# Performance work log

Measured on AMD Instinct MI355X. Metric: run time of the kernel, lower is better.

## Reference

```python
import jax, jax.numpy as jnp
import numpy as np

N_NODES = 20000
N_EDGES = 640000
IN_DIM = 128
HID = 128
NUM_GRAPHS = 64


def setup_inputs() -> dict:
    key = jax.random.key(0)
    ks = jax.random.split(key, 12)
    x = jax.random.normal(ks[0], (N_NODES, IN_DIM), dtype=jnp.float32)
    edge_index = jax.random.randint(ks[1], (2, N_EDGES), 0, N_NODES, dtype=jnp.int64)
    batch = jnp.sort(jax.random.randint(ks[2], (N_NODES,), 0, NUM_GRAPHS, dtype=jnp.int64))
    edge_attr = jax.random.uniform(ks[3], (N_EDGES,), dtype=jnp.float32)
    s1 = 1.0 / np.sqrt(IN_DIM)
    s2 = 1.0 / np.sqrt(HID)
    # GraphConv layer 1: lin_rel (with bias) on aggregated messages, lin_root (no bias) on x
    W1_rel = jax.random.uniform(ks[4], (HID, IN_DIM), minval=-s1, maxval=s1, dtype=jnp.float32)
    b1 = jax.random.uniform(ks[5], (HID,), minval=-s1, maxval=s1, dtype=jnp.float32)
    W1_root = jax.random.uniform(ks[6], (HID, IN_DIM), minval=-s1, maxval=s1, dtype=jnp.float32)
    # GraphConv layer 3 (conv2 is unused in forward)
    W3_rel = jax.random.uniform(ks[7], (HID, HID), minval=-s2, maxval=s2, dtype=jnp.float32)
    b3 = jax.random.uniform(ks[8], (HID,), minval=-s2, maxval=s2, dtype=jnp.float32)
    W3_root = jax.random.uniform(ks[9], (HID, HID), minval=-s2, maxval=s2, dtype=jnp.float32)
    # Final linear head
    Wlin = jax.random.uniform(ks[10], (1, HID), minval=-s2, maxval=s2, dtype=jnp.float32)
    blin = jax.random.uniform(ks[11], (1,), minval=-s2, maxval=s2, dtype=jnp.float32)
    return {
        "x": x, "edge_index": edge_index, "batch": batch, "edge_attr": edge_attr,
        "W1_rel": W1_rel, "b1": b1, "W1_root": W1_root,
        "W3_rel": W3_rel, "b3": b3, "W3_root": W3_root,
        "Wlin": Wlin, "blin": blin, "num_graphs": NUM_GRAPHS,
    }


def graph_conv(x, src, dst, edge_w, W_rel, b_rel, W_root):
    # PyG GraphConv (aggr='add'): out = W_rel @ sum_{j in N(i)} w_ij * x_j + b_rel + W_root @ x_i
    msg = x[src] * edge_w[:, None]                       # [E, d] gather + scale
    agg = jax.ops.segment_sum(msg, dst, num_segments=x.shape[0])  # [N, d] scatter-add
    return agg @ W_rel.T + b_rel + x @ W_root.T


def reference(x, edge_index, batch, edge_attr,
              W1_rel, b1, W1_root, W3_rel, b3, W3_root, Wlin, blin, num_graphs):
    src, dst = edge_index[0], edge_index[1]
    h = graph_conv(x, src, dst, edge_attr, W1_rel, b1, W1_root)
    h = jax.nn.relu(h)
    # dropout p=0.5 is identity in eval mode
    h = graph_conv(h, src, dst, edge_attr, W3_rel, b3, W3_root)
    # global_mean_pool over per-node graph ids
    sums = jax.ops.segment_sum(h, batch, num_segments=num_graphs)          # [G, H]
    counts = jax.ops.segment_sum(jnp.ones((h.shape[0],), h.dtype), batch,
                                 num_segments=num_graphs)                  # [G]
    pooled = sums / jnp.maximum(counts, 1.0)[:, None]
    out = jax.nn.relu(pooled @ Wlin.T + blin)                              # [G, 1]
    return out
```

## Files before the change

kernel.cpp:

```cpp
#include <hip/hip_runtime.h>

#define N_NODES 20000
#define N_EDGES 640000
#define DIM 128
#define NGRAPH 64
#define NBUCK 313
#define CAP 2560
#define EPB 1024
#define NB_PART 625
#define NB_WCONV 32
#define NB_GEMM 1252
#define RED_BLOCKS 512

typedef __attribute__((ext_vector_type(8))) short short8;
typedef __attribute__((ext_vector_type(4))) float floatx4;

__device__ __forceinline__ unsigned int bf16rne(float f) {
    unsigned int u = __float_as_uint(f);
    return (u + 0x7FFFu + ((u >> 16) & 1u)) >> 16;
}

__global__ __launch_bounds__(256) void k_part_prep(
    const int* __restrict__ src, const int* __restrict__ dst,
    const float* __restrict__ ew,
    const float* __restrict__ W1rel, const float* __restrict__ W1root,
    const float* __restrict__ W3rel, const float* __restrict__ W3root,
    const float* __restrict__ b3, const float* __restrict__ Wlin,
    int* __restrict__ gcursor, int2* __restrict__ part,
    unsigned short* __restrict__ wbh, unsigned short* __restrict__ wbl,
    float* __restrict__ vrel, float* __restrict__ vroot, float* __restrict__ cb3) {

    const int t = threadIdx.x;
    const int blk = blockIdx.x;

    if (blk < NB_PART) {
        __shared__ int lhist[NBUCK], lbase[NBUCK], gbase[NBUCK], lcur[NBUCK];
        __shared__ int2 lrec[EPB];
        for (int i = t; i < NBUCK; i += 256) lhist[i] = 0;
        __syncthreads();
        const int e0 = blk * EPB;
        const int tot = min(EPB, N_EDGES - e0);
        int mys[4], myd[4];
        float myw[4];
        for (int i = 0; i < 4; ++i) {
            int e = e0 + i * 256 + t;
            if (e < N_EDGES) {
                mys[i] = src[e];
                myd[i] = dst[e];
                myw[i] = ew[e];
                atomicAdd(&lhist[myd[i] >> 6], 1);
            } else {
                myd[i] = -1;
            }
        }
        __syncthreads();
        if (t < 64) {
            int carry = 0;
            for (int c = 0; c < 5; ++c) {
                int idx = c * 64 + t;
                int v = (idx < NBUCK) ? lhist[idx] : 0;
                int xv = v;
                for (int s = 1; s < 64; s <<= 1) {
                    int u = __shfl_up(xv, s);
                    if (t >= s) xv += u;
                }
                if (idx < NBUCK) { lbase[idx] = carry + xv - v; lcur[idx] = 0; }
                carry += __shfl(xv, 63);
            }
        }
        __syncthreads();
        for (int i = t; i < NBUCK; i += 256) {
            int cnt = lhist[i];
            gbase[i] = cnt ? (i * CAP + atomicAdd(&gcursor[i], cnt)) : 0;
        }
        __syncthreads();
        for (int i = 0; i < 4; ++i) {
            if (myd[i] >= 0) {
                int bb = myd[i] >> 6;
                int slot = lbase[bb] + atomicAdd(&lcur[bb], 1);
                lrec[slot] = make_int2((myd[i] << 16) | mys[i], __float_as_int(myw[i]));
            }
        }
        __syncthreads();
        for (int i = t; i < tot; i += 256) {
            int2 rc = lrec[i];
            int bb = ((unsigned)rc.x >> 16) >> 6;
            part[gbase[bb] + (i - lbase[bb])] = rc;
        }
    } else if (blk < NB_PART + NB_WCONV) {
        const int b = blk - NB_PART;
        for (int i = b * 256 + t; i < 256 * DIM; i += NB_WCONV * 256) {
            int n = i >> 7, k = i & 127;
            float v = (n < DIM) ? W1rel[n * DIM + k] : W1root[(n - DIM) * DIM + k];
            unsigned int h = bf16rne(v);
            wbh[i] = (unsigned short)h;
            wbl[i] = (unsigned short)bf16rne(v - __uint_as_float(h << 16));
        }
    } else {
        if (t < 64) {
            for (int kk = 0; kk < 2; ++kk) {
                int k = t + kk * 64;
                float sr = 0.f, so = 0.f;
                for (int h = 0; h < DIM; ++h) {
                    float wl = Wlin[h];
                    sr = fmaf(wl, W3rel[h * DIM + k], sr);
                    so = fmaf(wl, W3root[h * DIM + k], so);
                }
                vrel[k] = sr;
                vroot[k] = so;
            }
            float c = b3[t] * Wlin[t] + b3[t + 64] * Wlin[t + 64];
            for (int m = 32; m > 0; m >>= 1) c += __shfl_xor(c, m);
            if (t == 0) cb3[0] = c;
        }
    }
}

union SMem2 {
    struct { int2 lrec[CAP]; int nh[64], ncur[64]; } s;
    struct { unsigned short h[64 * DIM], l[64 * DIM]; } g;
};

__global__ __launch_bounds__(256) void k_sort_gemm(
    const int* __restrict__ gcursor, int2* __restrict__ part,
    int* __restrict__ off, int* __restrict__ nend,
    const float* __restrict__ x,
    const unsigned short* __restrict__ wbh, const unsigned short* __restrict__ wbl,
    const float* __restrict__ b1,
    unsigned short* __restrict__ yb, float* __restrict__ r) {
    __shared__ SMem2 sm;
    const int t = threadIdx.x;

    if (blockIdx.x < NBUCK) {
        const int b = blockIdx.x;
        const int base = b * CAP;
        const int cnt = gcursor[b];
        for (int i = t; i < cnt; i += 256) sm.s.lrec[i] = part[base + i];
        if (t < 64) sm.s.nh[t] = 0;
        __syncthreads();
        for (int i = t; i < cnt; i += 256)
            atomicAdd(&sm.s.nh[((unsigned)sm.s.lrec[i].x >> 16) & 63], 1);
        __syncthreads();
        if (t < 64) {
            int v = sm.s.nh[t];
            int xv = v;
            for (int s = 1; s < 64; s <<= 1) {
                int u = __shfl_up(xv, s);
                if (t >= s) xv += u;
            }
            int excl = xv - v;
            sm.s.ncur[t] = excl;
            int node = b * 64 + t;
            if (node < N_NODES) {
                off[node] = base + excl;
                nend[node] = base + excl + v;
            }
        }
        __syncthreads();
        for (int i = t; i < cnt; i += 256) {
            int2 rc = sm.s.lrec[i];
            int dl = ((unsigned)rc.x >> 16) & 63;
            int p = atomicAdd(&sm.s.ncur[dl], 1);
            part[base + p] = make_int2(rc.x & 0xFFFF, rc.y);
        }
    } else {
        const int tile = blockIdx.x - NBUCK;
        const int g = tile >> 2;
        const int col0 = (tile & 3) * 64;
        uint4* sh = (uint4*)sm.g.h;
        uint4* sl = (uint4*)sm.g.l;
        const uint4* gh = (const uint4*)wbh + (size_t)col0 * 16;
        const uint4* gl = (const uint4*)wbl + (size_t)col0 * 16;
        for (int i = t; i < 1024; i += 256) {
            int row = i >> 4, c = i & 15;
            int sc = row * 16 + (c ^ (row & 15));
            sh[sc] = gh[i];
            sl[sc] = gl[i];
        }
        __syncthreads();

        const int lane = t & 63;
        const int m = lane & 15;
        const int q = lane >> 4;
        const int row0 = g * 64 + (t >> 6) * 16;
        const int row = row0 + m;
        const bool ok = row < N_NODES;
        const short8* SH = (const short8*)sm.g.h;
        const short8* SL = (const short8*)sm.g.l;

        floatx4 acc[4];
        #pragma unroll
        for (int i = 0; i < 4; ++i) acc[i] = (floatx4)(0.f);

        #pragma unroll
        for (int kc = 0; kc < 4; ++kc) {
            float4 v0 = make_float4(0.f, 0.f, 0.f, 0.f);
            float4 v1 = make_float4(0.f, 0.f, 0.f, 0.f);
            if (ok) {
                const float4* xp = (const float4*)(x + (size_t)row * DIM + kc * 32 + q * 8);
                v0 = xp[0];
                v1 = xp[1];
            }
            float f[8] = {v0.x, v0.y, v0.z, v0.w, v1.x, v1.y, v1.z, v1.w};
            short8 ah, al;
            #pragma unroll
            for (int i = 0; i < 8; ++i) {
                unsigned int h = bf16rne(f[i]);
                ah[i] = (short)h;
                al[i] = (short)bf16rne(f[i] - __uint_as_float(h << 16));
            }
            #pragma unroll
            for (int nt = 0; nt < 4; ++nt) {
                int nl = nt * 16 + m;
                int cc = (kc * 4 + q) ^ m;
                short8 bh = SH[nl * 16 + cc];
                short8 bl = SL[nl * 16 + cc];
                acc[nt] = __builtin_amdgcn_mfma_f32_16x16x32_bf16(ah, bh, acc[nt], 0, 0, 0);
                acc[nt] = __builtin_amdgcn_mfma_f32_16x16x32_bf16(al, bh, acc[nt], 0, 0, 0);
                acc[nt] = __builtin_amdgcn_mfma_f32_16x16x32_bf16(ah, bl, acc[nt], 0, 0, 0);
            }
        }

        #pragma unroll
        for (int nt = 0; nt < 4; ++nt) {
            int col = col0 + nt * 16 + m;
            float bias = (col >= DIM) ? b1[col - DIM] : 0.f;
            #pragma unroll
            for (int reg = 0; reg < 4; ++reg) {
                int orow = row0 + q * 4 + reg;
                if (orow < N_NODES) {
                    float v = acc[nt][reg];
                    if (col < DIM)
                        yb[orow * DIM + col] = (unsigned short)bf16rne(v);
                    else
                        r[orow * DIM + (col - DIM)] = v + bias;
                }
            }
        }
    }
}

__global__ __launch_bounds__(256) void k_agg(const unsigned int* __restrict__ yb,
                                             const float2* __restrict__ r2,
                                             const int* __restrict__ off,
                                             const int* __restrict__ nend,
                                             const int2* __restrict__ grec,
                                             const float2* __restrict__ vrel2,
                                             const float2* __restrict__ vroot2,
                                             float* __restrict__ aout,
                                             float* __restrict__ bout) {
    const int lane = threadIdx.x & 63;
    const int node = blockIdx.x * 4 + (threadIdx.x >> 6);
    if (node >= N_NODES) return;

    int j = off[node];
    const int e1 = nend[node];
    float sx = 0.f, sy = 0.f;
    for (; j + 8 <= e1; j += 8) {
        int2 rc[8];
        #pragma unroll
        for (int u = 0; u < 8; ++u) rc[u] = grec[j + u];
        unsigned int v[8];
        #pragma unroll
        for (int u = 0; u < 8; ++u) v[u] = yb[rc[u].x * 64 + lane];
        #pragma unroll
        for (int u = 0; u < 8; ++u) {
            float w = __int_as_float(rc[u].y);
            sx = fmaf(w, __uint_as_float(v[u] << 16), sx);
            sy = fmaf(w, __uint_as_float(v[u] & 0xFFFF0000u), sy);
        }
    }
    for (; j < e1; ++j) {
        int2 rcs = grec[j];
        float w = __int_as_float(rcs.y);
        unsigned int vv = yb[rcs.x * 64 + lane];
        sx = fmaf(w, __uint_as_float(vv << 16), sx);
        sy = fmaf(w, __uint_as_float(vv & 0xFFFF0000u), sy);
    }
    float2 rr = r2[(size_t)node * 64 + lane];
    float hx = fmaxf(sx + rr.x, 0.f);
    float hy = fmaxf(sy + rr.y, 0.f);
    float2 vr = vrel2[lane];
    float2 vo = vroot2[lane];
    float pa = hx * vr.x + hy * vr.y;
    float pb = hx * vo.x + hy * vo.y;
    for (int mm = 32; mm > 0; mm >>= 1) {
        pa += __shfl_xor(pa, mm);
        pb += __shfl_xor(pb, mm);
    }
    if (lane == 0) {
        aout[node] = pa;
        bout[node] = pb;
    }
}

__global__ __launch_bounds__(256) void k_reduce_final(
    const int2* __restrict__ grec, const int* __restrict__ off,
    const int* __restrict__ nend,
    const float* __restrict__ a, const float* __restrict__ bvec,
    const int* __restrict__ batch,
    float* __restrict__ gpart, int* __restrict__ gpartc,
    int* __restrict__ ticket_red,
    const float* __restrict__ cb3, const float* __restrict__ blin,
    float* __restrict__ out) {
    __shared__ float sbin[NGRAPH];
    __shared__ int cbin[NGRAPH];
    __shared__ int islast;
    const int t = threadIdx.x;
    for (int i = t; i < NGRAPH; i += 256) { sbin[i] = 0.f; cbin[i] = 0; }
    __syncthreads();
    const int lane = t & 63;
    const int gw = blockIdx.x * 4 + (t >> 6);
    const int nw = gridDim.x * 4;
    for (int node = gw; node < N_NODES; node += nw) {
        const int e0 = off[node], e1 = nend[node];
        float s = 0.f;
        for (int j = e0 + lane; j < e1; j += 64) {
            int2 rc = grec[j];
            s = fmaf(__int_as_float(rc.y), a[rc.x], s);
        }
        for (int mm = 32; mm > 0; mm >>= 1) s += __shfl_xor(s, mm);
        if (lane == 0) {
            int g = batch[node];
            atomicAdd(&sbin[g], s + bvec[node]);
            atomicAdd(&cbin[g], 1);
        }
    }
    __syncthreads();
    const int slot = blockIdx.x & 63;
    for (int i = t; i < NGRAPH; i += 256) {
        atomicAdd(&gpart[slot * NGRAPH + i], sbin[i]);
        if (cbin[i]) atomicAdd(&gpartc[slot * NGRAPH + i], cbin[i]);
    }
    __syncthreads();
    if (t == 0) {
        __threadfence();
        islast = (atomicAdd(ticket_red, 1) == (int)gridDim.x - 1);
    }
    __syncthreads();
    if (islast) {
        __threadfence();
        if (t < NGRAPH) {
            float S = 0.f;
            int C = 0;
            for (int s2 = 0; s2 < 64; ++s2) {
                S += __hip_atomic_load(&gpart[s2 * NGRAPH + t], __ATOMIC_RELAXED,
                                       __HIP_MEMORY_SCOPE_AGENT);
                C += __hip_atomic_load(&gpartc[s2 * NGRAPH + t], __ATOMIC_RELAXED,
                                       __HIP_MEMORY_SCOPE_AGENT);
            }
            float denom = (C > 0) ? (float)C : 1.f;
            float v = (S + (float)C * cb3[0]) / denom + blin[0];
            out[t] = (v > 0.f) ? v : 0.f;
        }
    }
}

extern "C" void kernel_launch(void* const* d_in, const int* in_sizes, int n_in,
                              void* d_out, int out_size, void* d_ws, size_t ws_size,
                              hipStream_t stream) {
    const float* x = (const float*)d_in[0];
    const int* edge_index = (const int*)d_in[1];
    const int* src = edge_index;
    const int* dst = edge_index + N_EDGES;
    const int* batch = (const int*)d_in[2];
    const float* ew = (const float*)d_in[3];
    const float* W1rel = (const float*)d_in[4];
    const float* b1 = (const float*)d_in[5];
    const float* W1root = (const float*)d_in[6];
    const float* W3rel = (const float*)d_in[7];
    const float* b3 = (const float*)d_in[8];
    const float* W3root = (const float*)d_in[9];
    const float* Wlin = (const float*)d_in[10];
    const float* blin = (const float*)d_in[11];
    float* out = (float*)d_out;

    char* w = (char*)d_ws;
    size_t o = 0;
    auto alloc = [&](size_t bytes) -> void* {
        void* p = w + o;
        o += bytes;
        o = (o + 255) & ~(size_t)255;
        return p;
    };
    char* zbase = (char*)alloc((NBUCK + 1) * 4 + 64 * NGRAPH * 4 * 2);
    int* gcursor = (int*)zbase;
    int* ticket_red = gcursor + NBUCK;
    float* gpart = (float*)(zbase + (NBUCK + 1) * 4);
    int* gpartc = (int*)(zbase + (NBUCK + 1) * 4 + 64 * NGRAPH * 4);
    const size_t zbytes = (NBUCK + 1) * 4 + 64 * NGRAPH * 4 * 2;

    unsigned short* wbh = (unsigned short*)alloc((size_t)256 * DIM * 2);
    unsigned short* wbl = (unsigned short*)alloc((size_t)256 * DIM * 2);
    unsigned short* yb = (unsigned short*)alloc((size_t)N_NODES * DIM * 2);
    float* r = (float*)alloc((size_t)N_NODES * DIM * 4);
    int2* part = (int2*)alloc((size_t)NBUCK * CAP * 8);
    int* off = (int*)alloc((size_t)N_NODES * 4);
    int* nend = (int*)alloc((size_t)N_NODES * 4);
    float* a = (float*)alloc((size_t)N_NODES * 4);
    float* b = (float*)alloc((size_t)N_NODES * 4);
    float* vrel = (float*)alloc(DIM * 4);
    float* vroot = (float*)alloc(DIM * 4);
    float* cb3 = (float*)alloc(4);

    hipMemsetAsync(zbase, 0, zbytes, stream);

    k_part_prep<<<NB_PART + NB_WCONV + 1, 256, 0, stream>>>(
        src, dst, ew, W1rel, W1root, W3rel, W3root, b3, Wlin,
        gcursor, part, wbh, wbl, vrel, vroot, cb3);

    k_sort_gemm<<<NBUCK + NB_GEMM, 256, 0, stream>>>(
        gcursor, part, off, nend, x, wbh, wbl, b1, yb, r);

    k_agg<<<(N_NODES + 3) / 4, 256, 0, stream>>>(
        (const unsigned int*)yb, (const float2*)r, off, nend, part,
        (const float2*)vrel, (const float2*)vroot, a, b);

    k_reduce_final<<<RED_BLOCKS, 256, 0, stream>>>(
        part, off, nend, a, b, batch, gpart, gpartc, ticket_red, cb3, blin, out);
}
```

Before: 181.6 us.

## Aggregate raw bf16 features before layer-1 GEMM and fuse the dot reductions

New measurement: 222.6 us. 22.6% more time.

```diff
diff --git a/kernel.cpp b/kernel.cpp
--- a/kernel.cpp
+++ b/kernel.cpp
@@ -8,9 +8,8 @@
 #define CAP 2560
 #define EPB 1024
 #define NB_PART 625
+#define NB_XCONV 160
 #define NB_WCONV 32
-#define NB_GEMM 1252
-#define RED_BLOCKS 512
 
 typedef __attribute__((ext_vector_type(8))) short short8;
 typedef __attribute__((ext_vector_type(4))) float floatx4;
@@ -20,15 +19,27 @@
     return (u + 0x7FFFu + ((u >> 16) & 1u)) >> 16;
 }
 
+__device__ __forceinline__ int lowerb(const int* __restrict__ arr, int n, int v) {
+    int lo = 0, hi = n;
+    while (lo < hi) {
+        int mid = (lo + hi) >> 1;
+        if (arr[mid] < v) lo = mid + 1; else hi = mid;
+    }
+    return lo;
+}
+
 __global__ __launch_bounds__(256) void k_part_prep(
     const int* __restrict__ src, const int* __restrict__ dst,
-    const float* __restrict__ ew,
+    const float* __restrict__ ew, const float* __restrict__ x,
+    const int* __restrict__ batch,
     const float* __restrict__ W1rel, const float* __restrict__ W1root,
     const float* __restrict__ W3rel, const float* __restrict__ W3root,
     const float* __restrict__ b3, const float* __restrict__ Wlin,
     int* __restrict__ gcursor, int2* __restrict__ part,
+    unsigned int* __restrict__ xb32,
     unsigned short* __restrict__ wbh, unsigned short* __restrict__ wbl,
-    float* __restrict__ vrel, float* __restrict__ vroot, float* __restrict__ cb3) {
+    float* __restrict__ vrel, float* __restrict__ vroot, float* __restrict__ cb3,
+    int* __restrict__ cntg) {
 
     const int t = threadIdx.x;
     const int blk = blockIdx.x;
@@ -70,8 +81,8 @@
         }
         __syncthreads();
         for (int i = t; i < NBUCK; i += 256) {
-            int cnt = lhist[i];
-            gbase[i] = cnt ? (i * CAP + atomicAdd(&gcursor[i], cnt)) : 0;
+            int c = lhist[i];
+            gbase[i] = c ? (i * CAP + atomicAdd(&gcursor[i], c)) : 0;
         }
         __syncthreads();
         for (int i = 0; i < 4; ++i) {
@@ -87,8 +98,19 @@
             int bb = ((unsigned)rc.x >> 16) >> 6;
             part[gbase[bb] + (i - lbase[bb])] = rc;
         }
-    } else if (blk < NB_PART + NB_WCONV) {
+    } else if (blk < NB_PART + NB_XCONV) {
         const int b = blk - NB_PART;
+        const float4* x4 = (const float4*)x;
+        uint2* xh2 = (uint2*)xb32;
+        for (int i = b * 256 + t; i < N_NODES * 32; i += NB_XCONV * 256) {
+            float4 v = x4[i];
+            uint2 hp;
+            hp.x = bf16rne(v.x) | (bf16rne(v.y) << 16);
+            hp.y = bf16rne(v.z) | (bf16rne(v.w) << 16);
+            xh2[i] = hp;
+        }
+    } else if (blk < NB_PART + NB_XCONV + NB_WCONV) {
+        const int b = blk - (NB_PART + NB_XCONV);
         for (int i = b * 256 + t; i < 256 * DIM; i += NB_WCONV * 256) {
             int n = i >> 7, k = i & 127;
             float v = (n < DIM) ? W1rel[n * DIM + k] : W1root[(n - DIM) * DIM + k];
@@ -109,6 +131,7 @@
                 vrel[k] = sr;
                 vroot[k] = so;
             }
+            cntg[t] = lowerb(batch, N_NODES, t + 1) - lowerb(batch, N_NODES, t);
             float c = b3[t] * Wlin[t] + b3[t + 64] * Wlin[t + 64];
             for (int m = 32; m > 0; m >>= 1) c += __shfl_xor(c, m);
             if (t == 0) cb3[0] = c;
@@ -116,243 +139,241 @@
     }
 }
 
-union SMem2 {
-    struct { int2 lrec[CAP]; int nh[64], ncur[64]; } s;
-    struct { unsigned short h[64 * DIM], l[64 * DIM]; } g;
-};
-
-__global__ __launch_bounds__(256) void k_sort_gemm(
-    const int* __restrict__ gcursor, int2* __restrict__ part,
-    int* __restrict__ off, int* __restrict__ nend,
-    const float* __restrict__ x,
+__global__ __launch_bounds__(256) void k_zgather(
+    const int* __restrict__ gcursor, const int2* __restrict__ part,
+    const unsigned int* __restrict__ xb32, float* __restrict__ z) {
+    __shared__ int2 lrec[4][256];
+    __shared__ int lcur[4];
+    const int t = threadIdx.x;
+    const int w = t >> 6;
+    const int lane = t & 63;
+    const int nodeBase = blockIdx.x * 4;
+    const int bucket = nodeBase >> 6;
+
+    if (t < 4) lcur[t] = 0;
+    __syncthreads();
+    const int base = bucket * CAP;
+    const int cnt = min(gcursor[bucket], CAP);
+    for (int i = t; i < cnt; i += 256) {
+        int2 rc = part[base + i];
+        int wi = (int)((unsigned)rc.x >> 16) - nodeBase;
+        if ((unsigned)wi < 4u) {
+            int s = atomicAdd(&lcur[wi], 1);
+            if (s < 256) lrec[wi][s] = rc;
+        }
+    }
+    __syncthreads();
+
+    const int node = nodeBase + w;
+    if (node >= N_NODES) return;
+    const int len = min(lcur[w], 256);
+    float sx = 0.f, sy = 0.f;
+    int j = 0;
+    for (; j + 8 <= len; j += 8) {
+        int2 rc[8];
+        #pragma unroll
+        for (int u = 0; u < 8; ++u) rc[u] = lrec[w][j + u];
+        unsigned int v[8];
+        #pragma unroll
+        for (int u = 0; u < 8; ++u) v[u] = xb32[(size_t)(rc[u].x & 0xFFFF) * 64 + lane];
+        #pragma unroll
+        for (int u = 0; u < 8; ++u) {
+            float ww = __int_as_float(rc[u].y);
+            sx = fmaf(ww, __uint_as_float(v[u] << 16), sx);
+            sy = fmaf(ww, __uint_as_float(v[u] & 0xFFFF0000u), sy);
+        }
+    }
+    for (; j < len; ++j) {
+        int2 rc = lrec[w][j];
+        float ww = __int_as_float(rc.y);
+        unsigned int vv = xb32[(size_t)(rc.x & 0xFFFF) * 64 + lane];
+        sx = fmaf(ww, __uint_as_float(vv << 16), sx);
+        sy = fmaf(ww, __uint_as_float(vv & 0xFFFF0000u), sy);
+    }
+    float2* z2 = (float2*)z;
+    z2[(size_t)node * 64 + lane] = make_float2(sx, sy);
+}
+
+__global__ __launch_bounds__(256) void k_gemm_dots(
+    const float* __restrict__ x, const float* __restrict__ z,
     const unsigned short* __restrict__ wbh, const unsigned short* __restrict__ wbl,
     const float* __restrict__ b1,
-    unsigned short* __restrict__ yb, float* __restrict__ r) {
-    __shared__ SMem2 sm;
+    const float* __restrict__ vrel, const float* __restrict__ vroot,
+    const int* __restrict__ batch,
+    float* __restrict__ aArr, float* __restrict__ gsum) {
+    __shared__ unsigned short smem[2][128 * 32];
     const int t = threadIdx.x;
-
-    if (blockIdx.x < NBUCK) {
-        const int b = blockIdx.x;
-        const int base = b * CAP;
-        const int cnt = gcursor[b];
-        for (int i = t; i < cnt; i += 256) sm.s.lrec[i] = part[base + i];
-        if (t < 64) sm.s.nh[t] = 0;
-        __syncthreads();
-        for (int i = t; i < cnt; i += 256)
-            atomicAdd(&sm.s.nh[((unsigned)sm.s.lrec[i].x >> 16) & 63], 1);
-        __syncthreads();
-        if (t < 64) {
-            int v = sm.s.nh[t];
-            int xv = v;
-            for (int s = 1; s < 64; s <<= 1) {
-                int u = __shfl_up(xv, s);
-                if (t >= s) xv += u;
+    const int g = blockIdx.x;
+    const int c0 = blockIdx.y * 64;
+
+    const int lane = t & 63;
+    const int m = lane & 15;
+    const int q = lane >> 4;
+    const int row0 = g * 64 + (t >> 6) * 16;
+
+    floatx4 acc[4];
+    #pragma unroll
+    for (int i = 0; i < 4; ++i) acc[i] = (floatx4)(0.f);
+
+    uint4* sh4 = (uint4*)smem[0];
+    uint4* sl4 = (uint4*)smem[1];
+    const uint4* gh = (const uint4*)wbh;
+    const uint4* gl = (const uint4*)wbl;
+
+    for (int kc = 0; kc < 4; ++kc) {
+        __syncthreads();
+        for (int i = t; i < 512; i += 256) {
+            int row = i >> 2, ch = i & 3;
+            int wbrow = (row < 64) ? (c0 + row) : (128 + c0 + row - 64);
+            int sc = row * 4 + (ch ^ ((row >> 2) & 3));
+            int gi = wbrow * 16 + kc * 4 + ch;
+            sh4[sc] = gh[gi];
+            sl4[sc] = gl[gi];
+        }
+        __syncthreads();
+
+        const int arow = row0 + m;
+        const bool ok = arow < N_NODES;
+        const float* zp = z + (size_t)arow * DIM + kc * 32 + q * 8;
+        float4 z0 = ((const float4*)zp)[0];
+        float4 z1 = ((const float4*)zp)[1];
+        float4 x0 = make_float4(0.f, 0.f, 0.f, 0.f);
+        float4 x1 = make_float4(0.f, 0.f, 0.f, 0.f);
+        if (ok) {
+            const float* xp = x + (size_t)arow * DIM + kc * 32 + q * 8;
+            x0 = ((const float4*)xp)[0];
+            x1 = ((const float4*)xp)[1];
+        }
+        float zf[8] = {z0.x, z0.y, z0.z, z0.w, z1.x, z1.y, z1.z, z1.w};
+        float xf[8] = {x0.x, x0.y, x0.z, x0.w, x1.x, x1.y, x1.z, x1.w};
+        short8 zh, zl, xh, xl;
+        #pragma unroll
+        for (int i = 0; i < 8; ++i) {
+            unsigned int h = bf16rne(zf[i]);
+            zh[i] = (short)h;
+            zl[i] = (short)bf16rne(zf[i] - __uint_as_float(h << 16));
+            unsigned int h2 = bf16rne(xf[i]);
+            xh[i] = (short)h2;
+            xl[i] = (short)bf16rne(xf[i] - __uint_as_float(h2 << 16));
+        }
+
+        const short8* SH = (const short8*)smem[0];
+        const short8* SL = (const short8*)smem[1];
+        #pragma unroll
+        for (int nt = 0; nt < 4; ++nt) {
+            int rrel = nt * 16 + m;
+            int rroot = 64 + nt * 16 + m;
+            int cc1 = q ^ ((rrel >> 2) & 3);
+            int cc2 = q ^ ((rroot >> 2) & 3);
+            short8 bh = SH[rrel * 4 + cc1];
+            short8 bl = SL[rrel * 4 + cc1];
+            short8 ch = SH[rroot * 4 + cc2];
+            short8 cl = SL[rroot * 4 + cc2];
+            acc[nt] = __builtin_amdgcn_mfma_f32_16x16x32_bf16(zh, bh, acc[nt], 0, 0, 0);
+            acc[nt] = __builtin_amdgcn_mfma_f32_16x16x32_bf16(zl, bh, acc[nt], 0, 0, 0);
+            acc[nt] = __builtin_amdgcn_mfma_f32_16x16x32_bf16(zh, bl, acc[nt], 0, 0, 0);
+            acc[nt] = __builtin_amdgcn_mfma_f32_16x16x32_bf16(xh, ch, acc[nt], 0, 0, 0);
+            acc[nt] = __builtin_amdgcn_mfma_f32_16x16x32_bf16(xl, ch, acc[nt], 0, 0, 0);
+            acc[nt] = __builtin_amdgcn_mfma_f32_16x16x32_bf16(xh, cl, acc[nt], 0, 0, 0);
+        }
+    }
+
+    float pa[4] = {0.f, 0.f, 0.f, 0.f};
+    float pb[4] = {0.f, 0.f, 0.f, 0.f};
+    #pragma unroll
+    for (int nt = 0; nt < 4; ++nt) {
+        int col = c0 + nt * 16 + m;
+        float vb = b1[col];
+        float vr = vrel[col];
+        float vo = vroot[col];
+        #pragma unroll
+        for (int reg = 0; reg < 4; ++reg) {
+            float h = fmaxf(acc[nt][reg] + vb, 0.f);
+            pa[reg] = fmaf(h, vr, pa[reg]);
+            pb[reg] = fmaf(h, vo, pb[reg]);
+        }
+    }
+    #pragma unroll
+    for (int reg = 0; reg < 4; ++reg) {
+        for (int mask = 1; mask < 16; mask <<= 1) {
+            pa[reg] += __shfl_xor(pa[reg], mask);
+            pb[reg] += __shfl_xor(pb[reg], mask);
+        }
+    }
+    const int g_lo = batch[min(g * 64, N_NODES - 1)];
+    const int g_hi = batch[min(g * 64 + 63, N_NODES - 1)];
+    float s_lo = 0.f, s_hi = 0.f;
+    if (m == 0) {
+        #pragma unroll
+        for (int reg = 0; reg < 4; ++reg) {
+            int row = row0 + q * 4 + reg;
+            if (row < N_NODES) {
+                atomicAdd(&aArr[row], pa[reg]);
+                if (batch[row] == g_lo) s_lo += pb[reg];
+                else s_hi += pb[reg];
             }
-            int excl = xv - v;
-            sm.s.ncur[t] = excl;
-            int node = b * 64 + t;
-            if (node < N_NODES) {
-                off[node] = base + excl;
-                nend[node] = base + excl + v;
-            }
-        }
-        __syncthreads();
-        for (int i = t; i < cnt; i += 256) {
-            int2 rc = sm.s.lrec[i];
-            int dl = ((unsigned)rc.x >> 16) & 63;
-            int p = atomicAdd(&sm.s.ncur[dl], 1);
-            part[base + p] = make_int2(rc.x & 0xFFFF, rc.y);
-        }
-    } else {
-        const int tile = blockIdx.x - NBUCK;
-        const int g = tile >> 2;
-        const int col0 = (tile & 3) * 64;
-        uint4* sh = (uint4*)sm.g.h;
-        uint4* sl = (uint4*)sm.g.l;
-        const uint4* gh = (const uint4*)wbh + (size_t)col0 * 16;
-        const uint4* gl = (const uint4*)wbl + (size_t)col0 * 16;
-        for (int i = t; i < 1024; i += 256) {
-            int row = i >> 4, c = i & 15;
-            int sc = row * 16 + (c ^ (row & 15));
-            sh[sc] = gh[i];
-            sl[sc] = gl[i];
-        }
-        __syncthreads();
-
-        const int lane = t & 63;
-        const int m = lane & 15;
-        const int q = lane >> 4;
-        const int row0 = g * 64 + (t >> 6) * 16;
-        const int row = row0 + m;
-        const bool ok = row < N_NODES;
-        const short8* SH = (const short8*)sm.g.h;
-        const short8* SL = (const short8*)sm.g.l;
-
-        floatx4 acc[4];
-        #pragma unroll
-        for (int i = 0; i < 4; ++i) acc[i] = (floatx4)(0.f);
-
-        #pragma unroll
-        for (int kc = 0; kc < 4; ++kc) {
-            float4 v0 = make_float4(0.f, 0.f, 0.f, 0.f);
-            float4 v1 = make_float4(0.f, 0.f, 0.f, 0.f);
-            if (ok) {
-                const float4* xp = (const float4*)(x + (size_t)row * DIM + kc * 32 + q * 8);
-                v0 = xp[0];
-                v1 = xp[1];
-            }
-            float f[8] = {v0.x, v0.y, v0.z, v0.w, v1.x, v1.y, v1.z, v1.w};
-            short8 ah, al;
-            #pragma unroll
-            for (int i = 0; i < 8; ++i) {
-                unsigned int h = bf16rne(f[i]);
-                ah[i] = (short)h;
-                al[i] = (short)bf16rne(f[i] - __uint_as_float(h << 16));
-            }
-            #pragma unroll
-            for (int nt = 0; nt < 4; ++nt) {
-                int nl = nt * 16 + m;
-                int cc = (kc * 4 + q) ^ m;
-                short8 bh = SH[nl * 16 + cc];
-                short8 bl = SL[nl * 16 + cc];
-                acc[nt] = __builtin_amdgcn_mfma_f32_16x16x32_bf16(ah, bh, acc[nt], 0, 0, 0);
-                acc[nt] = __builtin_amdgcn_mfma_f32_16x16x32_bf16(al, bh, acc[nt], 0, 0, 0);
-                acc[nt] = __builtin_amdgcn_mfma_f32_16x16x32_bf16(ah, bl, acc[nt], 0, 0, 0);
-            }
-        }
-
-        #pragma unroll
-        for (int nt = 0; nt < 4; ++nt) {
-            int col = col0 + nt * 16 + m;
-            float bias = (col >= DIM) ? b1[col - DIM] : 0.f;
-            #pragma unroll
-            for (int reg = 0; reg < 4; ++reg) {
-                int orow = row0 + q * 4 + reg;
-                if (orow < N_NODES) {
-                    float v = acc[nt][reg];
-                    if (col < DIM)
-                        yb[orow * DIM + col] = (unsigned short)bf16rne(v);
-                    else
-                        r[orow * DIM + (col - DIM)] = v + bias;
-                }
-            }
-        }
-    }
-}
-
-__global__ __launch_bounds__(256) void k_agg(const unsigned int* __restrict__ yb,
-                                             const float2* __restrict__ r2,
-                                             const int* __restrict__ off,
-                                             const int* __restrict__ nend,
-                                             const int2* __restrict__ grec,
-                                             const float2* __restrict__ vrel2,
-                                             const float2* __restrict__ vroot2,
-                                             float* __restrict__ aout,
-                                             float* __restrict__ bout) {
-    const int lane = threadIdx.x & 63;
-    const int node = blockIdx.x * 4 + (threadIdx.x >> 6);
-    if (node >= N_NODES) return;
-
-    int j = off[node];
-    const int e1 = nend[node];
-    float sx = 0.f, sy = 0.f;
-    for (; j + 8 <= e1; j += 8) {
-        int2 rc[8];
-        #pragma unroll
-        for (int u = 0; u < 8; ++u) rc[u] = grec[j + u];
-        unsigned int v[8];
-        #pragma unroll
-        for (int u = 0; u < 8; ++u) v[u] = yb[rc[u].x * 64 + lane];
-        #pragma unroll
-        for (int u = 0; u < 8; ++u) {
-            float w = __int_as_float(rc[u].y);
-            sx = fmaf(w, __uint_as_float(v[u] << 16), sx);
-            sy = fmaf(w, __uint_as_float(v[u] & 0xFFFF0000u), sy);
-        }
-    }
-    for (; j < e1; ++j) {
-        int2 rcs = grec[j];
-        float w = __int_as_float(rcs.y);
-        unsigned int vv = yb[rcs.x * 64 + lane];
-        sx = fmaf(w, __uint_as_float(vv << 16), sx);
-        sy = fmaf(w, __uint_as_float(vv & 0xFFFF0000u), sy);
-    }
-    float2 rr = r2[(size_t)node * 64 + lane];
-    float hx = fmaxf(sx + rr.x, 0.f);
-    float hy = fmaxf(sy + rr.y, 0.f);
-    float2 vr = vrel2[lane];
-    float2 vo = vroot2[lane];
-    float pa = hx * vr.x + hy * vr.y;
-    float pb = hx * vo.x + hy * vo.y;
-    for (int mm = 32; mm > 0; mm >>= 1) {
-        pa += __shfl_xor(pa, mm);
-        pb += __shfl_xor(pb, mm);
+        }
+    }
+    for (int mask = 1; mask < 64; mask <<= 1) {
+        s_lo += __shfl_xor(s_lo, mask);
+        s_hi += __shfl_xor(s_hi, mask);
     }
     if (lane == 0) {
-        aout[node] = pa;
-        bout[node] = pb;
+        if (s_lo != 0.f) atomicAdd(&gsum[g_lo], s_lo);
+        if (g_hi != g_lo && s_hi != 0.f) atomicAdd(&gsum[g_hi], s_hi);
     }
 }
 
 __global__ __launch_bounds__(256) void k_reduce_final(
-    const int2* __restrict__ grec, const int* __restrict__ off,
-    const int* __restrict__ nend,
-    const float* __restrict__ a, const float* __restrict__ bvec,
-    const int* __restrict__ batch,
-    float* __restrict__ gpart, int* __restrict__ gpartc,
-    int* __restrict__ ticket_red,
+    const int2* __restrict__ part, const int* __restrict__ gcursor,
+    const float* __restrict__ aArr, const int* __restrict__ batch,
+    float* __restrict__ gsum, const int* __restrict__ cntg,
+    int* __restrict__ ticket,
     const float* __restrict__ cb3, const float* __restrict__ blin,
     float* __restrict__ out) {
-    __shared__ float sbin[NGRAPH];
-    __shared__ int cbin[NGRAPH];
-    __shared__ int islast;
+    __shared__ int sbatch[64];
+    __shared__ int flag;
     const int t = threadIdx.x;
-    for (int i = t; i < NGRAPH; i += 256) { sbin[i] = 0.f; cbin[i] = 0; }
+    const int b = blockIdx.x >> 2;
+    const int qtr = blockIdx.x & 3;
+    const int nb = b * 64;
+    if (t < 64) sbatch[t] = batch[min(nb + t, N_NODES - 1)];
     __syncthreads();
-    const int lane = t & 63;
-    const int gw = blockIdx.x * 4 + (t >> 6);
-    const int nw = gridDim.x * 4;
-    for (int node = gw; node < N_NODES; node += nw) {
-        const int e0 = off[node], e1 = nend[node];
-        float s = 0.f;
-        for (int j = e0 + lane; j < e1; j += 64) {
-            int2 rc = grec[j];
-            s = fmaf(__int_as_float(rc.y), a[rc.x], s);
-        }
-        for (int mm = 32; mm > 0; mm >>= 1) s += __shfl_xor(s, mm);
-        if (lane == 0) {
-            int g = batch[node];
-            atomicAdd(&sbin[g], s + bvec[node]);
-            atomicAdd(&cbin[g], 1);
-        }
-    }
-    __syncthreads();
-    const int slot = blockIdx.x & 63;
-    for (int i = t; i < NGRAPH; i += 256) {
-        atomicAdd(&gpart[slot * NGRAPH + i], sbin[i]);
-        if (cbin[i]) atomicAdd(&gpartc[slot * NGRAPH + i], cbin[i]);
+    const int g_lo = sbatch[0];
+    const int g_hi = sbatch[63];
+    const int base = b * CAP;
+    const int cnt = min(gcursor[b], CAP);
+    const int i0 = (cnt * qtr) >> 2;
+    const int i1 = (cnt * (qtr + 1)) >> 2;
+    float s_lo = 0.f, s_hi = 0.f;
+    for (int i = i0 + t; i < i1; i += 256) {
+        int2 rc = part[base + i];
+        float val = __int_as_float(rc.y) * aArr[rc.x & 0xFFFF];
+        int dl = (int)((unsigned)rc.x >> 16) - nb;
+        if (sbatch[dl] == g_lo) s_lo += val;
+        else s_hi += val;
+    }
+    for (int mask = 1; mask < 64; mask <<= 1) {
+        s_lo += __shfl_xor(s_lo, mask);
+        s_hi += __shfl_xor(s_hi, mask);
+    }
+    if ((t & 63) == 0) {
+        if (s_lo != 0.f) atomicAdd(&gsum[g_lo], s_lo);
+        if (g_hi != g_lo && s_hi != 0.f) atomicAdd(&gsum[g_hi], s_hi);
     }
     __syncthreads();
     if (t == 0) {
         __threadfence();
-        islast = (atomicAdd(ticket_red, 1) == (int)gridDim.x - 1);
+        flag = (atomicAdd(ticket, 1) == (int)gridDim.x - 1);
     }
     __syncthreads();
-    if (islast) {
+    if (flag && t < NGRAPH) {
         __threadfence();
-        if (t < NGRAPH) {
-            float S = 0.f;
-            int C = 0;
-            for (int s2 = 0; s2 < 64; ++s2) {
-                S += __hip_atomic_load(&gpart[s2 * NGRAPH + t], __ATOMIC_RELAXED,
-                                       __HIP_MEMORY_SCOPE_AGENT);
-                C += __hip_atomic_load(&gpartc[s2 * NGRAPH + t], __ATOMIC_RELAXED,
-                                       __HIP_MEMORY_SCOPE_AGENT);
-            }
-            float denom = (C > 0) ? (float)C : 1.f;
-            float v = (S + (float)C * cb3[0]) / denom + blin[0];
-            out[t] = (v > 0.f) ? v : 0.f;
-        }
+        float S = __hip_atomic_load(&gsum[t], __ATOMIC_RELAXED, __HIP_MEMORY_SCOPE_AGENT);
+        int C = cntg[t];
+        float denom = (C > 0) ? (float)C : 1.f;
+        float v = (S + (float)C * cb3[0]) / denom + blin[0];
+        out[t] = (v > 0.f) ? v : 0.f;
     }
 }
 
@@ -383,39 +404,34 @@
         o = (o + 255) & ~(size_t)255;
         return p;
     };
-    char* zbase = (char*)alloc((NBUCK + 1) * 4 + 64 * NGRAPH * 4 * 2);
+    const size_t zwords = NBUCK + 1 + NGRAPH + N_NODES;
+    char* zbase = (char*)alloc(zwords * 4);
     int* gcursor = (int*)zbase;
-    int* ticket_red = gcursor + NBUCK;
-    float* gpart = (float*)(zbase + (NBUCK + 1) * 4);
-    int* gpartc = (int*)(zbase + (NBUCK + 1) * 4 + 64 * NGRAPH * 4);
-    const size_t zbytes = (NBUCK + 1) * 4 + 64 * NGRAPH * 4 * 2;
-
+    int* ticket = gcursor + NBUCK;
+    float* gsum = (float*)(ticket + 1);
+    float* aArr = gsum + NGRAPH;
+
+    unsigned int* xb32 = (unsigned int*)alloc((size_t)20032 * 64 * 4);
     unsigned short* wbh = (unsigned short*)alloc((size_t)256 * DIM * 2);
     unsigned short* wbl = (unsigned short*)alloc((size_t)256 * DIM * 2);
-    unsigned short* yb = (unsigned short*)alloc((size_t)N_NODES * DIM * 2);
-    float* r = (float*)alloc((size_t)N_NODES * DIM * 4);
+    float* z = (float*)alloc((size_t)20032 * DIM * 4);
     int2* part = (int2*)alloc((size_t)NBUCK * CAP * 8);
-    int* off = (int*)alloc((size_t)N_NODES * 4);
-    int* nend = (int*)alloc((size_t)N_NODES * 4);
-    float* a = (float*)alloc((size_t)N_NODES * 4);
-    float* b = (float*)alloc((size_t)N_NODES * 4);
     float* vrel = (float*)alloc(DIM * 4);
     float* vroot = (float*)alloc(DIM * 4);
     float* cb3 = (float*)alloc(4);
-
-    hipMemsetAsync(zbase, 0, zbytes, stream);
-
-    k_part_prep<<<NB_PART + NB_WCONV + 1, 256, 0, stream>>>(
-        src, dst, ew, W1rel, W1root, W3rel, W3root, b3, Wlin,
-        gcursor, part, wbh, wbl, vrel, vroot, cb3);
-
-    k_sort_gemm<<<NBUCK + NB_GEMM, 256, 0, stream>>>(
-        gcursor, part, off, nend, x, wbh, wbl, b1, yb, r);
-
-    k_agg<<<(N_NODES + 3) / 4, 256, 0, stream>>>(
-        (const unsigned int*)yb, (const float2*)r, off, nend, part,
-        (const float2*)vrel, (const float2*)vroot, a, b);
-
-    k_reduce_final<<<RED_BLOCKS, 256, 0, stream>>>(
-        part, off, nend, a, b, batch, gpart, gpartc, ticket_red, cb3, blin, out);
-}
+    int* cntg = (int*)alloc(NGRAPH * 4);
+
+    hipMemsetAsync(zbase, 0, zwords * 4, stream);
+
+    k_part_prep<<<NB_PART + NB_XCONV + NB_WCONV + 1, 256, 0, stream>>>(
+        src, dst, ew, x, batch, W1rel, W1root, W3rel, W3root, b3, Wlin,
+        gcursor, part, xb32, wbh, wbl, vrel, vroot, cb3, cntg);
+
+    k_zgather<<<(N_NODES + 3) / 4, 256, 0, stream>>>(gcursor, part, xb32, z);
+
+    k_gemm_dots<<<dim3(NBUCK, 2), 256, 0, stream>>>(
+        x, z, wbh, wbl, b1, vrel, vroot, batch, aArr, gsum);
+
+    k_reduce_final<<<NBUCK * 4, 256, 0, stream>>>(
+        part, gcursor, aArr, batch, gsum, cntg, ticket, cb3, blin, out);
+}
```
